# Performance work log

Measured on AMD Instinct MI355X. Metric: run time of the kernel, lower is better.

The kernel has to match this reference:

```python
import jax, jax.numpy as jnp
import numpy as np

B, S, D, H, L, DFF = 32, 512, 1024, 16, 4, 2048
DK = D // H
NEG = -1e32
EPS = 1e-5


def setup_inputs() -> dict:
    key = jax.random.key(0)
    ks = jax.random.split(key, 8)
    std = 0.02
    inp = {
        "q_embed": jax.random.normal(ks[0], (B, S, D), jnp.float32),
        "qa_embed": jax.random.normal(ks[1], (B, S, D), jnp.float32),
        # per-block stacked params [L, ...]; torch Linear stored as [in, out]
        "Wk": jax.random.normal(ks[2], (L, D, D), jnp.float32) * std,
        "bk": jnp.zeros((L, D), jnp.float32),
        "Wv": jax.random.normal(ks[3], (L, D, D), jnp.float32) * std,
        "bv": jnp.zeros((L, D), jnp.float32),
        "Wo": jax.random.normal(ks[4], (L, D, D), jnp.float32) * std,
        "bo": jnp.zeros((L, D), jnp.float32),
        "ln1_s": jnp.ones((L, D), jnp.float32),
        "ln1_b": jnp.zeros((L, D), jnp.float32),
        "W1": jax.random.normal(ks[5], (L, D, DFF), jnp.float32) * std,
        "b1": jnp.zeros((L, DFF), jnp.float32),
        "W2": jax.random.normal(ks[6], (L, DFF, D), jnp.float32) * std,
        "b2": jnp.zeros((L, D), jnp.float32),
        "ln2_s": jnp.ones((L, D), jnp.float32),
        "ln2_b": jnp.zeros((L, D), jnp.float32),
    }
    return inp


def _ln(x, s, b):
    m = jnp.mean(x, axis=-1, keepdims=True)
    v = jnp.mean((x - m) ** 2, axis=-1, keepdims=True)
    return (x - m) / jnp.sqrt(v + EPS) * s + b


def _block(x, y, Wk, bk, Wv, bv, Wo, bo, l1s, l1b, W1, b1, W2, b2, l2s, l2b, allowed):
    # kq_same=1: q and k both use k_linear; q == k since query == key == x
    qk = (x @ Wk + bk).reshape(B, S, H, DK).transpose(0, 2, 1, 3)  # [B,H,S,DK]
    v = (y @ Wv + bv).reshape(B, S, H, DK).transpose(0, 2, 1, 3)
    scores = jnp.einsum("bhid,bhjd->bhij", qk, qk) / np.sqrt(DK)
    scores = jnp.where(allowed, scores, NEG)  # strictly-causal mask
    attn = jax.nn.softmax(scores, axis=-1)
    attn = attn * (jnp.arange(S)[None, None, :, None] > 0)  # zero_pad row 0
    o = jnp.einsum("bhij,bhjd->bhid", attn, v)  # [B,H,S,DK]
    o = o.transpose(0, 2, 1, 3).reshape(B, S, D) @ Wo + bo
    x = _ln(x + o, l1s, l1b)
    f = jax.nn.relu(x @ W1 + b1) @ W2 + b2
    return _ln(x + f, l2s, l2b)


def reference(q_embed, qa_embed, Wk, bk, Wv, bv, Wo, bo, ln1_s, ln1_b,
              W1, b1, W2, b2, ln2_s, ln2_b):
    allowed = jnp.tril(jnp.ones((S, S), bool), -1)  # j < i
    x, y = q_embed, qa_embed
    for i in range(L):
        x = _block(x, y, Wk[i], bk[i], Wv[i], bv[i], Wo[i], bo[i],
                   ln1_s[i], ln1_b[i], W1[i], b1[i], W2[i], b2[i],
                   ln2_s[i], ln2_b[i], allowed)
    return x
```

## Files before the change

### kernel.cpp

```cpp
#include <hip/hip_runtime.h>

#define B_ 32
#define S_ 512
#define D_ 1024
#define H_ 16
#define DK_ 64
#define DFF_ 2048
#define L_ 4

typedef __attribute__((ext_vector_type(8))) short short8;
typedef __attribute__((ext_vector_type(4))) float f32x4;
typedef unsigned short u16;
typedef unsigned int u32;
typedef __attribute__((ext_vector_type(4))) u16 u16x4;
typedef __attribute__((ext_vector_type(8))) u16 u16x8;

__device__ __forceinline__ u16 f2bf(float f) {
    u32 u = __float_as_uint(f);
    u = u + 0x7fffu + ((u >> 16) & 1u);
    return (u16)(u >> 16);
}
__device__ __forceinline__ u16 f2bf_t(float f) {
    return (u16)(__float_as_uint(f) >> 16);
}
__device__ __forceinline__ float bf2f(u16 v) {
    return __uint_as_float(((u32)v) << 16);
}

__device__ __forceinline__ void async16(const u16* g, u16* l) {
    __builtin_amdgcn_global_load_lds((const __attribute__((address_space(1))) u32*)g,
                                     (__attribute__((address_space(3))) u32*)l, 16, 0, 0);
}

template<int RELU, int OUTM>
__global__ __launch_bounds__(256, 2)
void gemm_kernel(const u16* __restrict__ A, const u16* __restrict__ Bt,
                 const float* __restrict__ bias, void* __restrict__ C,
                 int M, int N, int K)
{
    __shared__ __align__(16) u16 sA[128 * 32];
    __shared__ __align__(16) u16 sB[128 * 32];
    const int t = threadIdx.x;
    const int w = t >> 6, l = t & 63;
    const int lane16 = l & 15, quad = l >> 4;
    const int m0 = blockIdx.y * 128;
    const int n0 = blockIdx.x * 128;
    const int wm = (w >> 1) * 64;
    const int wn = (w & 1) * 64;

    f32x4 acc[4][4];
#pragma unroll
    for (int i = 0; i < 4; i++)
#pragma unroll
        for (int j = 0; j < 4; j++) acc[i][j] = f32x4{0.f, 0.f, 0.f, 0.f};

    int sa_r[2], sa_q[2];
#pragma unroll
    for (int i = 0; i < 2; i++) {
        int s = t + i * 256;
        int r = s >> 2;
        sa_r[i] = r;
        sa_q[i] = (s & 3) ^ ((r >> 1) & 3);
    }
    int ach[4], bch[4];
#pragma unroll
    for (int i = 0; i < 4; i++) {
        int ra = wm + i * 16 + lane16;
        ach[i] = (ra << 2) | (quad ^ ((ra >> 1) & 3));
        int rb = wn + i * 16 + lane16;
        bch[i] = (rb << 2) | (quad ^ ((rb >> 1) & 3));
    }

    const int niter = K >> 5;
    for (int kt = 0; kt < niter; kt++) {
        int k0 = kt << 5;
#pragma unroll
        for (int i = 0; i < 2; i++) {
            async16(A + (size_t)(m0 + sa_r[i]) * K + k0 + sa_q[i] * 8,
                    &sA[(size_t)(i * 256 + w * 64) * 8]);
            async16(Bt + (size_t)(n0 + sa_r[i]) * K + k0 + sa_q[i] * 8,
                    &sB[(size_t)(i * 256 + w * 64) * 8]);
        }
        __syncthreads();
        short8 af[4], bf[4];
#pragma unroll
        for (int i = 0; i < 4; i++) {
            af[i] = *(const short8*)&sA[ach[i] * 8];
            bf[i] = *(const short8*)&sB[bch[i] * 8];
        }
#pragma unroll
        for (int mi = 0; mi < 4; mi++)
#pragma unroll
            for (int ni = 0; ni < 4; ni++)
                acc[mi][ni] = __builtin_amdgcn_mfma_f32_16x16x32_bf16(
                    af[mi], bf[ni], acc[mi][ni], 0, 0, 0);
        __syncthreads();
    }

#pragma unroll
    for (int mi = 0; mi < 4; mi++) {
#pragma unroll
        for (int ni = 0; ni < 4; ni++) {
            int col = n0 + wn + ni * 16 + lane16;
            float bv = bias[col];
            if (OUTM == 2) {
                int tok0 = m0 + wm + mi * 16 + quad * 4;
                int bb = tok0 >> 9, s0 = tok0 & 511;
                int hh = col >> 6, dd = col & 63;
                u16x4 pk;
#pragma unroll
                for (int r2 = 0; r2 < 4; r2++) pk[r2] = f2bf(acc[mi][ni][r2] + bv);
                *(u16x4*)&((u16*)C)[(((size_t)bb * H_ + hh) * DK_ + dd) * S_ + s0] = pk;
            } else {
                int row = m0 + wm + mi * 16 + quad * 4;
#pragma unroll
                for (int r2 = 0; r2 < 4; r2++) {
                    float v = acc[mi][ni][r2] + bv;
                    if (RELU) v = fmaxf(v, 0.f);
                    size_t idx = (size_t)(row + r2) * N + col;
                    if (OUTM == 1) ((u16*)C)[idx] = f2bf(v);
                    else           ((float*)C)[idx] = v;
                }
            }
        }
    }
}

__global__ __launch_bounds__(256, 3)
void attn_kernel(const u16* __restrict__ qk, const u16* __restrict__ vt,
                 u16* __restrict__ ao)
{
    __shared__ __align__(16) u16 sP[4][32 * 72];
    const int t = threadIdx.x, w = t >> 6, l = t & 63;
    const int lane16 = l & 15, quad = l >> 4;
    const int p = blockIdx.x;
    const int bh = blockIdx.y;
    const int b = bh >> 4, h = bh & 15;
    const int band = (w < 2) ? (2 * p + w) : (15 - 2 * p - (w - 2));
    const int band0 = band * 32;
    const u16* kb = qk + (size_t)b * S_ * D_ + h * DK_;
    const u16* vb = vt + (size_t)bh * DK_ * S_;
    u16* aob = ao + (size_t)b * S_ * D_ + h * DK_;
    const float SC = 0.125f * 1.44269504f;
    u16* myP = sP[w];

    short8 bq[2][2];
#pragma unroll
    for (int ii = 0; ii < 2; ii++)
#pragma unroll
        for (int kf = 0; kf < 2; kf++)
            bq[ii][kf] = *(const short8*)(kb + (size_t)(band0 + ii * 16 + lane16) * D_ +
                                          kf * 32 + quad * 8);

    f32x4 aco[4][2];
    float lsum[2] = {0.f, 0.f};
#pragma unroll
    for (int di = 0; di < 4; di++)
#pragma unroll
        for (int ii = 0; ii < 2; ii++) aco[di][ii] = f32x4{0.f, 0.f, 0.f, 0.f};

    const int ntiles = (band >> 1) + 1;
    for (int jt = 0; jt < ntiles; jt++) {
        const int j0 = jt * 64;
        const bool diag = (jt == ntiles - 1);

        short8 aK[2][4];
#pragma unroll
        for (int kf = 0; kf < 2; kf++)
#pragma unroll
            for (int ji = 0; ji < 4; ji++)
                aK[kf][ji] = *(const short8*)(kb + (size_t)(j0 + ji * 16 + lane16) * D_ +
                                              kf * 32 + quad * 8);
        f32x4 sacc[4][2];
#pragma unroll
        for (int ji = 0; ji < 4; ji++)
#pragma unroll
            for (int ii = 0; ii < 2; ii++) sacc[ji][ii] = f32x4{0.f, 0.f, 0.f, 0.f};
#pragma unroll
        for (int kf = 0; kf < 2; kf++)
#pragma unroll
            for (int ji = 0; ji < 4; ji++)
#pragma unroll
                for (int ii = 0; ii < 2; ii++)
                    sacc[ji][ii] = __builtin_amdgcn_mfma_f32_16x16x32_bf16(
                        aK[kf][ji], bq[ii][kf], sacc[ji][ii], 0, 0, 0);

        short8 aV[2][4];
#pragma unroll
        for (int kf = 0; kf < 2; kf++)
#pragma unroll
            for (int di = 0; di < 4; di++)
                aV[kf][di] = *(const short8*)(vb + (size_t)(di * 16 + lane16) * S_ +
                                              j0 + kf * 32 + quad * 8);

#pragma unroll
        for (int ii = 0; ii < 2; ii++) {
#pragma unroll
            for (int ji = 0; ji < 4; ji++) {
                u16x4 pk;
#pragma unroll
                for (int r2 = 0; r2 < 4; r2++) {
                    float v = sacc[ji][ii][r2] * SC;
                    if (diag) {
                        int j = j0 + ji * 16 + quad * 4 + r2;
                        int i = band0 + ii * 16 + lane16;
                        if (j >= i) v = -3e38f;
                    }
                    float pv = exp2f(v);
                    lsum[ii] += pv;
                    pk[r2] = f2bf_t(pv);
                }
                *(u16x4*)&myP[(ii * 16 + lane16) * 72 + ji * 16 + quad * 4] = pk;
            }
        }

        short8 pf[2][2];
#pragma unroll
        for (int kf = 0; kf < 2; kf++)
#pragma unroll
            for (int ii = 0; ii < 2; ii++)
                pf[kf][ii] = *(const short8*)&myP[(ii * 16 + lane16) * 72 +
                                                  kf * 32 + quad * 8];
#pragma unroll
        for (int kf = 0; kf < 2; kf++)
#pragma unroll
            for (int di = 0; di < 4; di++)
#pragma unroll
                for (int ii = 0; ii < 2; ii++)
                    aco[di][ii] = __builtin_amdgcn_mfma_f32_16x16x32_bf16(
                        aV[kf][di], pf[kf][ii], aco[di][ii], 0, 0, 0);
    }

#pragma unroll
    for (int ii = 0; ii < 2; ii++) {
        lsum[ii] += __shfl_xor(lsum[ii], 16);
        lsum[ii] += __shfl_xor(lsum[ii], 32);
    }

#pragma unroll
    for (int ii = 0; ii < 2; ii++) {
        int row = band0 + ii * 16 + lane16;
        float lv = lsum[ii];
        float inv = (row == 0 || !(lv > 0.f)) ? 0.f : 1.f / lv;
#pragma unroll
        for (int di = 0; di < 4; di++) {
            u16x4 o;
#pragma unroll
            for (int r2 = 0; r2 < 4; r2++) o[r2] = f2bf(aco[di][ii][r2] * inv);
            *(u16x4*)&aob[(size_t)row * D_ + di * 16 + quad * 4] = o;
        }
    }
}

template<int XBF, int WF32>
__global__ __launch_bounds__(256)
void ln_kernel(const void* __restrict__ xin, const float* __restrict__ addv,
               const float* __restrict__ sc, const float* __restrict__ bi,
               u16* __restrict__ xb_out, float* __restrict__ f32_out)
{
    const int row = blockIdx.x;
    const int t = threadIdx.x;
    const int w = t >> 6, l = t & 63;
    __shared__ float red[8];
    f32x4 a;
    if (XBF) {
        u16x4 raw = ((const u16x4*)xin)[(size_t)row * 256 + t];
#pragma unroll
        for (int j = 0; j < 4; j++) a[j] = bf2f(raw[j]);
    } else {
        a = ((const f32x4*)xin)[(size_t)row * 256 + t];
    }
    f32x4 c = ((const f32x4*)(addv + (size_t)row * D_))[t];
    f32x4 v;
    float s1 = 0.f, s2 = 0.f;
#pragma unroll
    for (int j = 0; j < 4; j++) {
        v[j] = a[j] + c[j];
        s1 += v[j];
        s2 += v[j] * v[j];
    }
#pragma unroll
    for (int off = 32; off > 0; off >>= 1) {
        s1 += __shfl_xor(s1, off);
        s2 += __shfl_xor(s2, off);
    }
    if (l == 0) { red[w * 2] = s1; red[w * 2 + 1] = s2; }
    __syncthreads();
    s1 = red[0] + red[2] + red[4] + red[6];
    s2 = red[1] + red[3] + red[5] + red[7];
    float mean = s1 * (1.f / D_);
    float var = s2 * (1.f / D_) - mean * mean;
    float rstd = rsqrtf(var + 1e-5f);
    f32x4 s4 = ((const f32x4*)sc)[t];
    f32x4 b4 = ((const f32x4*)bi)[t];
    f32x4 o;
    u16x4 ob;
#pragma unroll
    for (int j = 0; j < 4; j++) {
        o[j] = (v[j] - mean) * rstd * s4[j] + b4[j];
        ob[j] = f2bf(o[j]);
    }
    ((u16x4*)(xb_out + (size_t)row * D_))[t] = ob;
    if (WF32) ((f32x4*)(f32_out + (size_t)row * D_))[t] = o;
}

__global__ void cvt_kernel(const float* __restrict__ in, u16* __restrict__ out, int n4)
{
    int i = blockIdx.x * blockDim.x + threadIdx.x;
    if (i < n4) {
        f32x4 v = ((const f32x4*)in)[i];
        u16x4 o;
#pragma unroll
        for (int j = 0; j < 4; j++) o[j] = f2bf(v[j]);
        ((u16x4*)out)[i] = o;
    }
}

__device__ __forceinline__ void tconv_body(const float* W, u16* WT, int K, int N,
                                           int bx, int by, int t)
{
    __shared__ float tile[64][65];
    const int n0 = bx * 64, k0 = by * 64;
#pragma unroll
    for (int i = 0; i < 4; i++) {
        int kr = (t >> 4) + i * 16;
        int nc = (t & 15) * 4;
        f32x4 v = *(const f32x4*)&W[(size_t)(k0 + kr) * N + n0 + nc];
        tile[kr][nc] = v[0]; tile[kr][nc + 1] = v[1];
        tile[kr][nc + 2] = v[2]; tile[kr][nc + 3] = v[3];
    }
    __syncthreads();
#pragma unroll
    for (int i = 0; i < 4; i++) {
        int nr = (t >> 4) + i * 16;
        int kc = (t & 15) * 4;
        u16x4 o;
#pragma unroll
        for (int j = 0; j < 4; j++) o[j] = f2bf(tile[kc + j][nr]);
        *(u16x4*)&WT[(size_t)(n0 + nr) * K + k0 + kc] = o;
    }
}

__global__ __launch_bounds__(256)
void wconv_kernel(const float* __restrict__ Wk, const float* __restrict__ Wv,
                  const float* __restrict__ Wo, const float* __restrict__ W1f,
                  const float* __restrict__ W2f,
                  u16* __restrict__ wk, u16* __restrict__ wv, u16* __restrict__ wo,
                  u16* __restrict__ w1, u16* __restrict__ w2)
{
    const int idx = blockIdx.x;
    const float* W; u16* T; int K, N, bx, by;
    if (idx < 768) {
        int wsel = idx >> 8, t16 = idx & 255;
        W = (wsel == 0) ? Wk : (wsel == 1) ? Wv : Wo;
        T = (wsel == 0) ? wk : (wsel == 1) ? wv : wo;
        K = 1024; N = 1024; bx = t16 & 15; by = t16 >> 4;
    } else if (idx < 1280) {
        int i = idx - 768;
        W = W1f; T = w1; K = 1024; N = 2048; bx = i & 31; by = i >> 5;
    } else {
        int i = idx - 1280;
        W = W2f; T = w2; K = 2048; N = 1024; bx = i & 15; by = i >> 4;
    }
    tconv_body(W, T, K, N, bx, by, threadIdx.x);
}

extern "C" void kernel_launch(void* const* d_in, const int* in_sizes, int n_in,
                              void* d_out, int out_size, void* d_ws, size_t ws_size,
                              hipStream_t stream)
{
    const float* q_embed = (const float*)d_in[0];
    const float* qa_embed = (const float*)d_in[1];
    const float* Wk = (const float*)d_in[2];
    const float* bk = (const float*)d_in[3];
    const float* Wv = (const float*)d_in[4];
    const float* bv = (const float*)d_in[5];
    const float* Wo = (const float*)d_in[6];
    const float* bo = (const float*)d_in[7];
    const float* ln1_s = (const float*)d_in[8];
    const float* ln1_b = (const float*)d_in[9];
    const float* W1 = (const float*)d_in[10];
    const float* b1 = (const float*)d_in[11];
    const float* W2 = (const float*)d_in[12];
    const float* b2 = (const float*)d_in[13];
    const float* ln2_s = (const float*)d_in[14];
    const float* ln2_b = (const float*)d_in[15];
    (void)in_sizes; (void)n_in; (void)out_size;

    char* ws = (char*)d_ws;
    size_t off = 0;
    auto carve = [&](size_t bytes) -> char* {
        char* p = ws + off;
        off += (bytes + 255) & ~(size_t)255;
        return p;
    };
    const size_t NTOK = (size_t)B_ * S_;
    u16* wk = (u16*)carve((size_t)D_ * D_ * 2);
    u16* wv = (u16*)carve((size_t)D_ * D_ * 2);
    u16* wo = (u16*)carve((size_t)D_ * D_ * 2);
    u16* w1 = (u16*)carve((size_t)D_ * DFF_ * 2);
    u16* w2 = (u16*)carve((size_t)DFF_ * D_ * 2);
    u16* x = (u16*)carve(NTOK * D_ * 2);
    u16* U12 = (u16*)carve(NTOK * DFF_ * 2);
    u16* U3 = (u16*)carve(NTOK * D_ * 2);
    size_t off_overlay = off;
    u16* ybf_sep = (u16*)carve(NTOK * D_ * 2);
    bool sep = (ws_size >= off);
    if (!sep) off = off_overlay;
    if (ws_size < off) return;

    u16* qkb = U12;
    u16* vbf = U12 + NTOK * D_;
    u16* hb = U12;
    u16* aob = U3;
    u16* ybf = sep ? ybf_sep : U3;
    float* of32 = (float*)d_out;

    cvt_kernel<<<16384, 256, 0, stream>>>(q_embed, x, (int)(NTOK * D_ / 4));
    if (sep)
        cvt_kernel<<<16384, 256, 0, stream>>>(qa_embed, ybf, (int)(NTOK * D_ / 4));

    const dim3 g1024(8, 128), g2048(16, 128);
    for (int lyr = 0; lyr < L_; lyr++) {
        const size_t wsq = (size_t)lyr * D_ * D_;
        const size_t wf1 = (size_t)lyr * D_ * DFF_;
        wconv_kernel<<<1792, 256, 0, stream>>>(Wk + wsq, Wv + wsq, Wo + wsq,
                                               W1 + wf1, W2 + wf1,
                                               wk, wv, wo, w1, w2);
        if (!sep)
            cvt_kernel<<<16384, 256, 0, stream>>>(qa_embed, ybf, (int)(NTOK * D_ / 4));
        gemm_kernel<0, 1><<<g1024, 256, 0, stream>>>(x, wk, bk + lyr * D_,
                                                     qkb, (int)NTOK, D_, D_);
        gemm_kernel<0, 2><<<g1024, 256, 0, stream>>>(ybf, wv, bv + lyr * D_,
                                                     vbf, (int)NTOK, D_, D_);
        attn_kernel<<<dim3(4, B_ * H_), 256, 0, stream>>>(qkb, vbf, aob);
        gemm_kernel<0, 0><<<g1024, 256, 0, stream>>>(aob, wo, bo + lyr * D_,
                                                     of32, (int)NTOK, D_, D_);
        if (lyr == 0)
            ln_kernel<0, 0><<<(int)NTOK, 256, 0, stream>>>(q_embed, of32,
                ln1_s + lyr * D_, ln1_b + lyr * D_, x, nullptr);
        else
            ln_kernel<1, 0><<<(int)NTOK, 256, 0, stream>>>(x, of32,
                ln1_s + lyr * D_, ln1_b + lyr * D_, x, nullptr);
        gemm_kernel<1, 1><<<g2048, 256, 0, stream>>>(x, w1, b1 + lyr * DFF_,
                                                     hb, (int)NTOK, DFF_, D_);
        gemm_kernel<0, 0><<<g1024, 256, 0, stream>>>(hb, w2, b2 + lyr * D_,
                                                     of32, (int)NTOK, D_, DFF_);
        if (lyr == L_ - 1)
            ln_kernel<1, 1><<<(int)NTOK, 256, 0, stream>>>(x, of32,
                ln2_s + lyr * D_, ln2_b + lyr * D_, x, (float*)d_out);
        else
            ln_kernel<1, 0><<<(int)NTOK, 256, 0, stream>>>(x, of32,
                ln2_s + lyr * D_, ln2_b + lyr * D_, x, nullptr);
    }
}
```

Measured before the change: 2.124 ms.

## Replace GEMM with 256x256 tiled, double-buffered, XCD-remapped pipelined kernel

Swaps the 128x128, single-buffered GEMM for a 256x256 tile kernel with 8 waves and a K-step of 64. It double-buffers global-to-LDS async loads across four MFMA phases, using an XOR-swizzled LDS layout, s_setprio around the MFMA bursts, and explicit vmcnt waits. Workgroup IDs are remapped so neighbouring tiles land on the same XCD for better L2 reuse. The goal is to raise arithmetic intensity and overlap memory with compute. The cost is a large 128KB LDS footprint, heavy register use, and fewer, larger tiles, which could hurt occupancy or wave balance.

Measured after the change: 1.798 ms. 15.3% less time.

```diff
diff --git a/kernel.cpp b/kernel.cpp
--- a/kernel.cpp
+++ b/kernel.cpp
@@ -32,79 +32,128 @@
                                      (__attribute__((address_space(3))) u32*)l, 16, 0, 0);
 }
 
+#define READ_A(P)                                                              \
+    afr[0][0] = *(const short8*)&lds[cb + arow + (2*(P)+0)*1024 + chv0];       \
+    afr[0][1] = *(const short8*)&lds[cb + arow + (2*(P)+0)*1024 + chv1];       \
+    afr[1][0] = *(const short8*)&lds[cb + arow + (2*(P)+1)*1024 + chv0];       \
+    afr[1][1] = *(const short8*)&lds[cb + arow + (2*(P)+1)*1024 + chv1];
+
+#define MFMA_PHASE(P)                                                          \
+    __builtin_amdgcn_s_barrier();                                              \
+    asm volatile("s_waitcnt lgkmcnt(0)" ::: "memory");                         \
+    __builtin_amdgcn_sched_barrier(0);                                         \
+    __builtin_amdgcn_s_setprio(1);                                             \
+    _Pragma("unroll")                                                          \
+    for (int mi2 = 0; mi2 < 2; mi2++) {                                        \
+        _Pragma("unroll")                                                      \
+        for (int ni = 0; ni < 4; ni++) {                                       \
+            acc[2*(P)+mi2][ni] = __builtin_amdgcn_mfma_f32_16x16x32_bf16(      \
+                afr[mi2][0], bfr[ni][0], acc[2*(P)+mi2][ni], 0, 0, 0);         \
+            acc[2*(P)+mi2][ni] = __builtin_amdgcn_mfma_f32_16x16x32_bf16(      \
+                afr[mi2][1], bfr[ni][1], acc[2*(P)+mi2][ni], 0, 0, 0);         \
+        }                                                                      \
+    }                                                                          \
+    __builtin_amdgcn_s_setprio(0);
+
 template<int RELU, int OUTM>
-__global__ __launch_bounds__(256, 2)
-void gemm_kernel(const u16* __restrict__ A, const u16* __restrict__ Bt,
-                 const float* __restrict__ bias, void* __restrict__ C,
-                 int M, int N, int K)
-{
-    __shared__ __align__(16) u16 sA[128 * 32];
-    __shared__ __align__(16) u16 sB[128 * 32];
+__global__ __launch_bounds__(512, 2)
+void gemm256(const u16* __restrict__ A, const u16* __restrict__ Bt,
+             const float* __restrict__ bias, void* __restrict__ C,
+             int M, int N, int K)
+{
+    __shared__ __align__(16) u16 lds[65536];
     const int t = threadIdx.x;
     const int w = t >> 6, l = t & 63;
     const int lane16 = l & 15, quad = l >> 4;
-    const int m0 = blockIdx.y * 128;
-    const int n0 = blockIdx.x * 128;
-    const int wm = (w >> 1) * 64;
-    const int wn = (w & 1) * 64;
-
-    f32x4 acc[4][4];
-#pragma unroll
-    for (int i = 0; i < 4; i++)
+    const int wm = w >> 2, wn = w & 3;
+
+    const int gx = gridDim.x;
+    const int nwg = gx * gridDim.y;
+    const int orig = blockIdx.y * gx + blockIdx.x;
+    const int q8 = nwg >> 3, r8 = nwg & 7;
+    const int xcd = orig & 7, sidx = orig >> 3;
+    const int nid = (xcd < r8 ? xcd * (q8 + 1) : r8 * (q8 + 1) + (xcd - r8) * q8) + sidx;
+    const int m0 = (nid / gx) * 256;
+    const int n0 = (nid % gx) * 256;
+
+    f32x4 acc[8][4];
+#pragma unroll
+    for (int i = 0; i < 8; i++)
 #pragma unroll
         for (int j = 0; j < 4; j++) acc[i][j] = f32x4{0.f, 0.f, 0.f, 0.f};
 
-    int sa_r[2], sa_q[2];
-#pragma unroll
-    for (int i = 0; i < 2; i++) {
-        int s = t + i * 256;
-        int r = s >> 2;
-        sa_r[i] = r;
-        sa_q[i] = (s & 3) ^ ((r >> 1) & 3);
-    }
-    int ach[4], bch[4];
-#pragma unroll
-    for (int i = 0; i < 4; i++) {
-        int ra = wm + i * 16 + lane16;
-        ach[i] = (ra << 2) | (quad ^ ((ra >> 1) & 3));
-        int rb = wn + i * 16 + lane16;
-        bch[i] = (rb << 2) | (quad ^ ((rb >> 1) & 3));
-    }
-
-    const int niter = K >> 5;
-    for (int kt = 0; kt < niter; kt++) {
-        int k0 = kt << 5;
-#pragma unroll
-        for (int i = 0; i < 2; i++) {
-            async16(A + (size_t)(m0 + sa_r[i]) * K + k0 + sa_q[i] * 8,
-                    &sA[(size_t)(i * 256 + w * 64) * 8]);
-            async16(Bt + (size_t)(n0 + sa_r[i]) * K + k0 + sa_q[i] * 8,
-                    &sB[(size_t)(i * 256 + w * 64) * 8]);
+    const int lr = l >> 3;
+    const int xorcol = ((l & 7) ^ lr) * 8;
+    const int aw8 = (w < 4 ? w * 8 : 128 + (w - 4) * 8);
+    const u16* Asrc = A + (size_t)(m0 + aw8 + lr) * K + xorcol;
+    const u16* Bsrc = Bt + (size_t)(n0 + w * 8 + lr) * K + xorcol;
+
+    auto stageA = [&](int tile, int q) {
+        const int c = tile & 1;
+        async16(Asrc + (size_t)(q * 32) * K + (tile << 6),
+                &lds[c * 16384 + (aw8 + q * 32) * 64]);
+    };
+    auto stageB = [&](int tile, int j) {
+        const int c = tile & 1;
+        async16(Bsrc + (size_t)(j * 64) * K + (tile << 6),
+                &lds[32768 + c * 16384 + (j * 64 + w * 8) * 64]);
+    };
+
+    const int chv0 = ((0 + quad) ^ (lane16 & 7)) * 8;
+    const int chv1 = ((4 + quad) ^ (lane16 & 7)) * 8;
+    const int arow = (wm * 128 + lane16) * 64;
+    const int brow = 32768 + (wn * 64 + lane16) * 64;
+
+    const int NT = K >> 6;
+
+    stageA(0, 0); stageB(0, 0); stageB(0, 1);
+    stageA(0, 1); stageB(0, 2); stageB(0, 3);
+    stageA(0, 2);
+    stageA(0, 3);
+    stageA(1, 0); stageB(1, 0); stageB(1, 1);
+    stageA(1, 1); stageB(1, 2); stageB(1, 3);
+    stageA(1, 2);
+    asm volatile("s_waitcnt vmcnt(7)" ::: "memory");
+    __builtin_amdgcn_sched_barrier(0);
+    __builtin_amdgcn_s_barrier();
+
+    for (int tt = 0; tt < NT; tt++) {
+        const int cb = (tt & 1) * 16384;
+        short8 bfr[4][2], afr[2][2];
+        if (tt + 1 < NT) stageA(tt + 1, 3);
+#pragma unroll
+        for (int ni = 0; ni < 4; ni++) {
+            bfr[ni][0] = *(const short8*)&lds[cb + brow + ni * 1024 + chv0];
+            bfr[ni][1] = *(const short8*)&lds[cb + brow + ni * 1024 + chv1];
         }
-        __syncthreads();
-        short8 af[4], bf[4];
-#pragma unroll
-        for (int i = 0; i < 4; i++) {
-            af[i] = *(const short8*)&sA[ach[i] * 8];
-            bf[i] = *(const short8*)&sB[bch[i] * 8];
-        }
-#pragma unroll
-        for (int mi = 0; mi < 4; mi++)
-#pragma unroll
-            for (int ni = 0; ni < 4; ni++)
-                acc[mi][ni] = __builtin_amdgcn_mfma_f32_16x16x32_bf16(
-                    af[mi], bf[ni], acc[mi][ni], 0, 0, 0);
-        __syncthreads();
-    }
-
-#pragma unroll
-    for (int mi = 0; mi < 4; mi++) {
+        READ_A(0)
+        MFMA_PHASE(0)
+        __builtin_amdgcn_s_barrier();
+        if (tt + 2 < NT) { stageA(tt + 2, 0); stageB(tt + 2, 0); stageB(tt + 2, 1); }
+        READ_A(1)
+        MFMA_PHASE(1)
+        __builtin_amdgcn_s_barrier();
+        if (tt + 2 < NT) { stageA(tt + 2, 1); stageB(tt + 2, 2); stageB(tt + 2, 3); }
+        READ_A(2)
+        MFMA_PHASE(2)
+        __builtin_amdgcn_s_barrier();
+        if (tt + 2 < NT) stageA(tt + 2, 2);
+        READ_A(3)
+        MFMA_PHASE(3)
+        if (tt + 2 < NT) asm volatile("s_waitcnt vmcnt(7)" ::: "memory");
+        else             asm volatile("s_waitcnt vmcnt(0)" ::: "memory");
+        __builtin_amdgcn_sched_barrier(0);
+        __builtin_amdgcn_s_barrier();
+    }
+
+#pragma unroll
+    for (int mi = 0; mi < 8; mi++) {
 #pragma unroll
         for (int ni = 0; ni < 4; ni++) {
-            int col = n0 + wn + ni * 16 + lane16;
+            int col = n0 + wn * 64 + ni * 16 + lane16;
             float bv = bias[col];
             if (OUTM == 2) {
-                int tok0 = m0 + wm + mi * 16 + quad * 4;
+                int tok0 = m0 + wm * 128 + mi * 16 + quad * 4;
                 int bb = tok0 >> 9, s0 = tok0 & 511;
                 int hh = col >> 6, dd = col & 63;
                 u16x4 pk;
@@ -112,7 +161,7 @@
                 for (int r2 = 0; r2 < 4; r2++) pk[r2] = f2bf(acc[mi][ni][r2] + bv);
                 *(u16x4*)&((u16*)C)[(((size_t)bb * H_ + hh) * DK_ + dd) * S_ + s0] = pk;
             } else {
-                int row = m0 + wm + mi * 16 + quad * 4;
+                int row = m0 + wm * 128 + mi * 16 + quad * 4;
 #pragma unroll
                 for (int r2 = 0; r2 < 4; r2++) {
                     float v = acc[mi][ni][r2] + bv;
@@ -420,7 +469,7 @@
     if (sep)
         cvt_kernel<<<16384, 256, 0, stream>>>(qa_embed, ybf, (int)(NTOK * D_ / 4));
 
-    const dim3 g1024(8, 128), g2048(16, 128);
+    const dim3 G1024(4, 64), G2048(8, 64);
     for (int lyr = 0; lyr < L_; lyr++) {
         const size_t wsq = (size_t)lyr * D_ * D_;
         const size_t wf1 = (size_t)lyr * D_ * DFF_;
@@ -429,23 +478,23 @@
                                                wk, wv, wo, w1, w2);
         if (!sep)
             cvt_kernel<<<16384, 256, 0, stream>>>(qa_embed, ybf, (int)(NTOK * D_ / 4));
-        gemm_kernel<0, 1><<<g1024, 256, 0, stream>>>(x, wk, bk + lyr * D_,
-                                                     qkb, (int)NTOK, D_, D_);
-        gemm_kernel<0, 2><<<g1024, 256, 0, stream>>>(ybf, wv, bv + lyr * D_,
-                                                     vbf, (int)NTOK, D_, D_);
+        gemm256<0, 1><<<G1024, 512, 0, stream>>>(x, wk, bk + lyr * D_,
+                                                 qkb, (int)NTOK, D_, D_);
+        gemm256<0, 2><<<G1024, 512, 0, stream>>>(ybf, wv, bv + lyr * D_,
+                                                 vbf, (int)NTOK, D_, D_);
         attn_kernel<<<dim3(4, B_ * H_), 256, 0, stream>>>(qkb, vbf, aob);
-        gemm_kernel<0, 0><<<g1024, 256, 0, stream>>>(aob, wo, bo + lyr * D_,
-                                                     of32, (int)NTOK, D_, D_);
+        gemm256<0, 0><<<G1024, 512, 0, stream>>>(aob, wo, bo + lyr * D_,
+                                                 of32, (int)NTOK, D_, D_);
         if (lyr == 0)
             ln_kernel<0, 0><<<(int)NTOK, 256, 0, stream>>>(q_embed, of32,
                 ln1_s + lyr * D_, ln1_b + lyr * D_, x, nullptr);
         else
             ln_kernel<1, 0><<<(int)NTOK, 256, 0, stream>>>(x, of32,
                 ln1_s + lyr * D_, ln1_b + lyr * D_, x, nullptr);
-        gemm_kernel<1, 1><<<g2048, 256, 0, stream>>>(x, w1, b1 + lyr * DFF_,
-                                                     hb, (int)NTOK, DFF_, D_);
-        gemm_kernel<0, 0><<<g1024, 256, 0, stream>>>(hb, w2, b2 + lyr * D_,
-                                                     of32, (int)NTOK, D_, DFF_);
+        gemm256<1, 1><<<G2048, 512, 0, stream>>>(x, w1, b1 + lyr * DFF_,
+                                                 hb, (int)NTOK, DFF_, D_);
+        gemm256<0, 0><<<G1024, 512, 0, stream>>>(hb, w2, b2 + lyr * D_,
+                                                 of32, (int)NTOK, D_, DFF_);
         if (lyr == L_ - 1)
             ln_kernel<1, 1><<<(int)NTOK, 256, 0, stream>>>(x, of32,
                 ln2_s + lyr * D_, ln2_b + lyr * D_, x, (float*)d_out);
```
